# Performance work log

Hardware: AMD Instinct MI355X
Metric: run time of the kernel (lower is better)

Reference implementation:

```python
import jax, jax.numpy as jnp
import numpy as np

DIM = 1024
FF = 4096
BATCH = 4
SEQ = 2048
EPS = 1e-5


def setup_inputs() -> dict:
    key = jax.random.key(0)
    ks = jax.random.split(key, 8)
    x = jax.random.normal(ks[0], (BATCH, SEQ, DIM), dtype=jnp.float32)
    # phazor init: exp(2j*pi*arange(dim)/dim) * |randn(dim)|
    ang = 2.0 * np.pi * jnp.arange(DIM, dtype=jnp.float32) / DIM
    mag = jnp.abs(jax.random.normal(ks[1], (DIM,), dtype=jnp.float32))
    phazor_re = mag * jnp.cos(ang)
    phazor_im = mag * jnp.sin(ang)
    last_re = jax.random.normal(ks[2], (DIM,), dtype=jnp.float32)
    last_im = jax.random.normal(ks[3], (DIM,), dtype=jnp.float32)
    w1 = jax.random.normal(ks[4], (FF, DIM), dtype=jnp.float32) * DIM ** -0.5
    b1 = jnp.zeros((FF,), dtype=jnp.float32)
    w2 = jax.random.normal(ks[5], (DIM, FF), dtype=jnp.float32) * FF ** -0.5
    b2 = jnp.zeros((DIM,), dtype=jnp.float32)
    return {
        'x': x,
        'ln1_w': jnp.ones((DIM,), jnp.float32), 'ln1_b': jnp.zeros((DIM,), jnp.float32),
        'ln2_w': jnp.ones((DIM,), jnp.float32), 'ln2_b': jnp.zeros((DIM,), jnp.float32),
        'sc_lin': jnp.ones((DIM,), jnp.float32),
        'phazor_re': phazor_re, 'phazor_im': phazor_im,
        'last_re': last_re, 'last_im': last_im,
        'w1': w1, 'b1': b1, 'w2': w2, 'b2': b2,
    }


def _layer_norm(x, w, b):
    mu = jnp.mean(x, axis=-1, keepdims=True)
    var = jnp.mean(jnp.square(x - mu), axis=-1, keepdims=True)
    return (x - mu) * jax.lax.rsqrt(var + EPS) * w + b


def _sconv(x, phazor_re, phazor_im, last_re, last_im):
    B, L, D = x.shape
    dtype = x.dtype
    xc = x.astype(jnp.complex64)
    p_raw = phazor_re + 1j * phazor_im
    # tanh(|p|) * exp(i*angle(p))
    p = (jnp.tanh(jnp.abs(p_raw)) * jnp.exp(1j * jnp.angle(p_raw))).astype(jnp.complex64)
    t = jnp.arange(L)[:, None]
    prog = jnp.power(p[None, :], t)            # [L, D] complex
    filt_fft = jnp.fft.fft(prog, n=2 * L, axis=0)   # [2L, D]
    x_fft = jnp.fft.fft(xc, n=2 * L, axis=1)        # [B, 2L, D]
    conv = jnp.fft.ifft(filt_fft[None] * x_fft, axis=1)[:, :L]  # [B, L, D]
    last = (last_re + 1j * last_im)[None, None, :]  # [1,1,D] broadcast over batch
    conv_with_past = conv + last * prog[None] * p[None, None]
    return conv_with_past.real.astype(dtype)


def reference(x, ln1_w, ln1_b, ln2_w, ln2_b, sc_lin,
              phazor_re, phazor_im, last_re, last_im,
              w1, b1, w2, b2):
    # SConv branch
    x_res = x
    h = _layer_norm(x, ln1_w, ln1_b)
    h = jax.nn.silu(h)
    h = _sconv(h, phazor_re, phazor_im, last_re, last_im)
    h = h * sc_lin
    x = h + x_res
    # FFN branch
    x_res = x
    h = _layer_norm(x, ln2_w, ln2_b)
    h = jax.nn.silu(jnp.einsum('bld,fd->blf', h, w1) + b1)
    h = jnp.einsum('blf,df->bld', h, w2) + b2
    return h + x_res
```

## Files before the change

kernel.cpp:

```cpp
#include <hip/hip_runtime.h>
#include <cmath>


#define DIMD 1024
#define FFD  4096
#define BATCH 4
#define SEQL 2048
#define MROWS (BATCH*SEQL)
#define EPSF 1e-5f
#define CHUNKS 32
#define CLEN (SEQL/CHUNKS)

typedef __attribute__((ext_vector_type(8)))  _Float16 half8;
typedef __attribute__((ext_vector_type(4)))  _Float16 half4;
typedef __attribute__((ext_vector_type(4)))  float    floatx4;
typedef __attribute__((ext_vector_type(16))) float    floatx16;

#define ST_OFF   0u
#define E_OFF    33554432u
#define SIN_OFF  34603008u
#define H2_OFF   35651584u
#define W1H_OFF  52428800u
#define W2H_OFF  60817408u
#define Y1_OFF   69206016u

__device__ __forceinline__ void load_lds16(const _Float16* g, _Float16* l) {
    __builtin_amdgcn_global_load_lds(
        (const __attribute__((address_space(1))) unsigned int*)g,
        (__attribute__((address_space(3))) unsigned int*)l,
        16, 0, 0);
}

__global__ __launch_bounds__(256)
void cast_f32_f16(const float* __restrict__ src, _Float16* __restrict__ dst) {
    int i = (blockIdx.x * 256 + threadIdx.x) * 4;
    float4 v = *(const float4*)(src + i);
    half4 o;
    o.x = (_Float16)v.x; o.y = (_Float16)v.y; o.z = (_Float16)v.z; o.w = (_Float16)v.w;
    *(half4*)(dst + i) = o;
}

__global__ __launch_bounds__(256)
void ln_stats(const float* __restrict__ x, float2* __restrict__ st) {
    const size_t row = blockIdx.x;
    const int tid = threadIdx.x;
    float4 v = *(const float4*)(x + row * DIMD + tid * 4);
    float s = (v.x + v.y) + (v.z + v.w);
    float q = (v.x * v.x + v.y * v.y) + (v.z * v.z + v.w * v.w);
    #pragma unroll
    for (int off = 32; off; off >>= 1) {
        s += __shfl_down(s, off, 64);
        q += __shfl_down(q, off, 64);
    }
    __shared__ float red[8];
    if (!(tid & 63)) { red[tid >> 6] = s; red[4 + (tid >> 6)] = q; }
    __syncthreads();
    if (tid == 0) {
        s = (red[0] + red[1]) + (red[2] + red[3]);
        q = (red[4] + red[5]) + (red[6] + red[7]);
        const float mu = s * (1.f / DIMD);
        const float rs = rsqrtf(q * (1.f / DIMD) - mu * mu + EPSF);
        st[row] = make_float2(mu, rs);
    }
}

__global__ __launch_bounds__(256)
void ln_kernel(const float* __restrict__ x, const float* __restrict__ w,
               const float* __restrict__ b, _Float16* __restrict__ oh) {
    const size_t row = blockIdx.x;
    const int tid = threadIdx.x;
    float4 v = *(const float4*)(x + row * DIMD + tid * 4);
    float s = (v.x + v.y) + (v.z + v.w);
    float q = (v.x * v.x + v.y * v.y) + (v.z * v.z + v.w * v.w);
    #pragma unroll
    for (int off = 32; off; off >>= 1) {
        s += __shfl_down(s, off, 64);
        q += __shfl_down(q, off, 64);
    }
    __shared__ float red[8];
    if (!(tid & 63)) { red[tid >> 6] = s; red[4 + (tid >> 6)] = q; }
    __syncthreads();
    s = (red[0] + red[1]) + (red[2] + red[3]);
    q = (red[4] + red[5]) + (red[6] + red[7]);
    const float mu = s * (1.f / DIMD);
    const float rs = rsqrtf(q * (1.f / DIMD) - mu * mu + EPSF);
    float4 wv = *(const float4*)(w + tid * 4);
    float4 bv = *(const float4*)(b + tid * 4);
    half4 hv;
    hv.x = (_Float16)((v.x - mu) * rs * wv.x + bv.x);
    hv.y = (_Float16)((v.y - mu) * rs * wv.y + bv.y);
    hv.z = (_Float16)((v.z - mu) * rs * wv.z + bv.z);
    hv.w = (_Float16)((v.w - mu) * rs * wv.w + bv.w);
    *(half4*)(oh + row * DIMD + tid * 4) = hv;
}

__device__ __forceinline__ void get_p(const float* pre, const float* pim, int d,
                                      float& pr, float& pi) {
    float re = pre[d], im = pim[d];
    float r = sqrtf(re * re + im * im);
    float t = tanhf(r) / fmaxf(r, 1e-30f);
    pr = re * t; pi = im * t;
}

__device__ __forceinline__ float ln_silu(float xv, float2 st, float wd, float bd) {
    float o = (xv - st.x) * st.y * wd + bd;
    return o / (1.f + __expf(-o));
}

__global__ __launch_bounds__(256)
void scan_partial(const float* __restrict__ x, const float2* __restrict__ st,
                  const float* __restrict__ lw, const float* __restrict__ lb,
                  const float* __restrict__ pre, const float* __restrict__ pim,
                  float2* __restrict__ e) {
    const int d = blockIdx.x * 256 + threadIdx.x;
    const int c = blockIdx.y;
    const int bb = blockIdx.z;
    float pr, pi; get_p(pre, pim, d, pr, pi);
    const float wd = lw[d], bd = lb[d];
    float sr = 0.f, si = 0.f;
    const size_t row0 = (size_t)bb * SEQL + (size_t)c * CLEN;
    #pragma unroll 4
    for (int j = 0; j < CLEN; ++j) {
        float xv = x[(row0 + j) * DIMD + d];
        float2 sj = st[row0 + j];
        float hv = ln_silu(xv, sj, wd, bd);
        float nr = pr * sr - pi * si + hv;
        float ni = pr * si + pi * sr;
        sr = nr; si = ni;
    }
    e[((size_t)bb * CHUNKS + c) * DIMD + d] = make_float2(sr, si);
}

__global__ __launch_bounds__(256)
void scan_combine(const float2* __restrict__ e, const float* __restrict__ pre,
                  const float* __restrict__ pim, const float* __restrict__ lre,
                  const float* __restrict__ lim, float2* __restrict__ sv) {
    const int d = blockIdx.x * 256 + threadIdx.x;
    const int bb = blockIdx.y;
    float pr, pi; get_p(pre, pim, d, pr, pi);
    float qr = pr, qi = pi;
    #pragma unroll
    for (int s = 0; s < 6; ++s) {
        float nr = qr * qr - qi * qi;
        float ni = 2.f * qr * qi;
        qr = nr; qi = ni;
    }
    float sr = lre[d], si = lim[d];
    for (int c = 0; c < CHUNKS; ++c) {
        sv[((size_t)bb * CHUNKS + c) * DIMD + d] = make_float2(sr, si);
        float2 ec = e[((size_t)bb * CHUNKS + c) * DIMD + d];
        float nr = qr * sr - qi * si + ec.x;
        float ni = qr * si + qi * sr + ec.y;
        sr = nr; si = ni;
    }
}

__global__ __launch_bounds__(256)
void scan_final(const float* __restrict__ x, const float2* __restrict__ st,
                const float* __restrict__ lw, const float* __restrict__ lb,
                const float* __restrict__ pre, const float* __restrict__ pim,
                const float* __restrict__ sc, const float2* __restrict__ sv,
                float* __restrict__ x2) {
    const int d = blockIdx.x * 256 + threadIdx.x;
    const int c = blockIdx.y;
    const int bb = blockIdx.z;
    float pr, pi; get_p(pre, pim, d, pr, pi);
    const float wd = lw[d], bd = lb[d];
    float2 s0 = sv[((size_t)bb * CHUNKS + c) * DIMD + d];
    float sr = s0.x, si = s0.y;
    const float scd = sc[d];
    const size_t row0 = (size_t)bb * SEQL + (size_t)c * CLEN;
    #pragma unroll 4
    for (int j = 0; j < CLEN; ++j) {
        float xv = x[(row0 + j) * DIMD + d];
        float2 sj = st[row0 + j];
        float hv = ln_silu(xv, sj, wd, bd);
        float nr = pr * sr - pi * si + hv;
        float ni = pr * si + pi * sr;
        sr = nr; si = ni;
        x2[(row0 + j) * DIMD + d] = xv + scd * sr;
    }
}

#define GBM 128
#define GBN 128
#define GBK 64

template<int NCOLS>
__global__ __launch_bounds__(256)
void gemm1_32(const _Float16* __restrict__ A, const _Float16* __restrict__ W,
              const float* __restrict__ bias, _Float16* __restrict__ out_h,
              int N, int K) {
    __shared__ _Float16 As[GBM * GBK];
    __shared__ _Float16 Bs[GBN * GBK];
    const int tid  = threadIdx.x;
    const int lane = tid & 63;
    const int wave = tid >> 6;
    const int wm = (wave >> 1) * 64;
    const int wn = (wave & 1) * 64;
    const int n  = blockIdx.y * gridDim.x + blockIdx.x;
    const int xc = n & 7, ii = n >> 3;
    const size_t m0 = (size_t)(xc + ((ii / NCOLS) << 3)) * GBM;
    const size_t n0 = (size_t)(ii % NCOLS) * GBN;
    const int r32 = lane & 31;
    const int kg  = lane >> 5;

    const int srow = wave * 32 + (lane >> 3);
    const int ccp  = ((lane & 7) ^ (lane >> 3)) * 8;
    const _Float16* ag = A + (m0 + srow) * (size_t)K + ccp;
    const _Float16* wg = W + (n0 + srow) * (size_t)K + ccp;
    _Float16* asl = &As[(wave * 32) * GBK];
    _Float16* bsl = &Bs[(wave * 32) * GBK];

    floatx16 acc[2][2] = {};

    for (int k0 = 0; k0 < K; k0 += GBK) {
        #pragma unroll
        for (int t = 0; t < 4; ++t) {
            load_lds16(ag + k0 + (size_t)(t * 8) * K, asl + t * 8 * GBK);
            load_lds16(wg + k0 + (size_t)(t * 8) * K, bsl + t * 8 * GBK);
        }
        __syncthreads();
        #pragma unroll
        for (int ks = 0; ks < 4; ++ks) {
            const int slot = (((ks << 1) | kg) ^ (r32 & 7)) * 8;
            half8 af0 = *(const half8*)(&As[(wm +      r32) * GBK + slot]);
            half8 af1 = *(const half8*)(&As[(wm + 32 + r32) * GBK + slot]);
            half8 bf0 = *(const half8*)(&Bs[(wn +      r32) * GBK + slot]);
            half8 bf1 = *(const half8*)(&Bs[(wn + 32 + r32) * GBK + slot]);
            acc[0][0] = __builtin_amdgcn_mfma_f32_32x32x16_f16(af0, bf0, acc[0][0], 0, 0, 0);
            acc[0][1] = __builtin_amdgcn_mfma_f32_32x32x16_f16(af0, bf1, acc[0][1], 0, 0, 0);
            acc[1][0] = __builtin_amdgcn_mfma_f32_32x32x16_f16(af1, bf0, acc[1][0], 0, 0, 0);
            acc[1][1] = __builtin_amdgcn_mfma_f32_32x32x16_f16(af1, bf1, acc[1][1], 0, 0, 0);
        }
        __syncthreads();
    }

    #pragma unroll
    for (int ib = 0; ib < 2; ++ib) {
        #pragma unroll
        for (int jb = 0; jb < 2; ++jb) {
            const size_t gn = n0 + wn + jb * 32 + r32;
            const float bb = bias[gn];
            #pragma unroll
            for (int r = 0; r < 16; ++r) {
                const size_t gm = m0 + wm + ib * 32 + (r & 3) + 8 * (r >> 2) + 4 * kg;
                float v = acc[ib][jb][r] + bb;
                float sl = v / (1.f + __expf(-v));
                out_h[gm * (size_t)N + gn] = (_Float16)sl;
            }
        }
    }
}

template<int NCOLS>
__global__ __launch_bounds__(256)
void gemm2_16(const _Float16* __restrict__ A, const _Float16* __restrict__ W,
              const float* __restrict__ bias, const float* __restrict__ resid,
              float* __restrict__ out_f, int N, int K) {
    __shared__ _Float16 As[GBM * GBK];
    __shared__ _Float16 Bs[GBN * GBK];
    const int tid  = threadIdx.x;
    const int lane = tid & 63;
    const int wave = tid >> 6;
    const int wm = (wave >> 1) * 64;
    const int wn = (wave & 1) * 64;
    const int n  = blockIdx.y * gridDim.x + blockIdx.x;
    const int xc = n & 7, ii = n >> 3;
    const size_t m0 = (size_t)(xc + ((ii / NCOLS) << 3)) * GBM;
    const size_t n0 = (size_t)(ii % NCOLS) * GBN;
    const int fr = lane & 15;
    const int quad = lane >> 4;

    const int srow = wave * 32 + (lane >> 3);
    const int ccp  = ((lane & 7) ^ (lane >> 3)) * 8;
    const _Float16* ag = A + (m0 + srow) * (size_t)K + ccp;
    const _Float16* wg = W + (n0 + srow) * (size_t)K + ccp;
    _Float16* asl = &As[(wave * 32) * GBK];
    _Float16* bsl = &Bs[(wave * 32) * GBK];

    floatx4 acc[4][4] = {};

    for (int k0 = 0; k0 < K; k0 += GBK) {
        #pragma unroll
        for (int t = 0; t < 4; ++t) {
            load_lds16(ag + k0 + (size_t)(t * 8) * K, asl + t * 8 * GBK);
            load_lds16(wg + k0 + (size_t)(t * 8) * K, bsl + t * 8 * GBK);
        }
        __syncthreads();
        #pragma unroll
        for (int kk = 0; kk < GBK; kk += 32) {
            half8 af[4], bf[4];
            #pragma unroll
            for (int i = 0; i < 4; ++i) {
                const int slot = (((kk >> 3) + quad) ^ (fr & 7)) * 8;
                af[i] = *(const half8*)(&As[(wm + i * 16 + fr) * GBK + slot]);
                bf[i] = *(const half8*)(&Bs[(wn + i * 16 + fr) * GBK + slot]);
            }
            #pragma unroll
            for (int i = 0; i < 4; ++i)
                #pragma unroll
                for (int j = 0; j < 4; ++j)
                    acc[i][j] = __builtin_amdgcn_mfma_f32_16x16x32_f16(
                        af[i], bf[j], acc[i][j], 0, 0, 0);
        }
        __syncthreads();
    }

    #pragma unroll
    for (int i = 0; i < 4; ++i) {
        #pragma unroll
        for (int j = 0; j < 4; ++j) {
            #pragma unroll
            for (int r = 0; r < 4; ++r) {
                const size_t gm = m0 + wm + i * 16 + quad * 4 + r;
                const size_t gn = n0 + wn + j * 16 + fr;
                float v = acc[i][j][r] + bias[gn];
                out_f[gm * (size_t)N + gn] = v + resid[gm * (size_t)N + gn];
            }
        }
    }
}

extern "C" void kernel_launch(void* const* d_in, const int* in_sizes, int n_in,
                              void* d_out, int out_size, void* d_ws, size_t ws_size,
                              hipStream_t stream) {
    const float* x    = (const float*)d_in[0];
    const float* ln1w = (const float*)d_in[1];
    const float* ln1b = (const float*)d_in[2];
    const float* ln2w = (const float*)d_in[3];
    const float* ln2b = (const float*)d_in[4];
    const float* sc   = (const float*)d_in[5];
    const float* pre  = (const float*)d_in[6];
    const float* pim  = (const float*)d_in[7];
    const float* lre  = (const float*)d_in[8];
    const float* lim  = (const float*)d_in[9];
    const float* w1   = (const float*)d_in[10];
    const float* b1   = (const float*)d_in[11];
    const float* w2   = (const float*)d_in[12];
    const float* b2   = (const float*)d_in[13];

    char* ws = (char*)d_ws;
    float2*     st  = (float2*)(ws + ST_OFF);
    float2*     e   = (float2*)(ws + E_OFF);
    float2*     sv  = (float2*)(ws + SIN_OFF);
    _Float16*   h2  = (_Float16*)(ws + H2_OFF);
    _Float16*   w1h = (_Float16*)(ws + W1H_OFF);
    _Float16*   w2h = (_Float16*)(ws + W2H_OFF);
    _Float16*   y1  = (_Float16*)(ws + Y1_OFF);
    float*      x2  = (float*)d_out;
    float*      outp = (float*)d_out;

    cast_f32_f16<<<dim3(FFD * DIMD / 1024), 256, 0, stream>>>(w1, w1h);
    cast_f32_f16<<<dim3(FFD * DIMD / 1024), 256, 0, stream>>>(w2, w2h);
    ln_stats<<<dim3(MROWS), 256, 0, stream>>>(x, st);
    scan_partial<<<dim3(DIMD / 256, CHUNKS, BATCH), 256, 0, stream>>>(
        x, st, ln1w, ln1b, pre, pim, e);
    scan_combine<<<dim3(DIMD / 256, BATCH), 256, 0, stream>>>(
        e, pre, pim, lre, lim, sv);
    scan_final<<<dim3(DIMD / 256, CHUNKS, BATCH), 256, 0, stream>>>(
        x, st, ln1w, ln1b, pre, pim, sc, sv, x2);
    ln_kernel<<<dim3(MROWS), 256, 0, stream>>>(x2, ln2w, ln2b, h2);
    gemm1_32<32><<<dim3(FFD / GBN, MROWS / GBM), 256, 0, stream>>>(
        h2, w1h, b1, y1, FFD, DIMD);
    gemm2_16<8><<<dim3(DIMD / GBN, MROWS / GBM), 256, 0, stream>>>(
        y1, w2h, b2, x2, outp, DIMD, FFD);
}
```

Baseline: 353.7 us.

## Merge prep kernels and fold scan combine into final scan pass

The two weight-cast kernels and the LN-stats kernel become one launch, with each block picking its job from its index. The separate scan_combine kernel is removed. Each scan_final block now recomputes its chunk's starting state by walking the earlier chunk carries itself. This removes two kernel launches and the write/read round-trip of the intermediate state buffer, in exchange for redundant carry computation (up to 31 steps per block).

```diff
diff --git a/kernel.cpp b/kernel.cpp
--- a/kernel.cpp
+++ b/kernel.cpp
@@ -10,6 +10,7 @@
 #define EPSF 1e-5f
 #define CHUNKS 32
 #define CLEN (SEQL/CHUNKS)
+#define CAST_BLKS (FFD*DIMD/1024)
 
 typedef __attribute__((ext_vector_type(8)))  _Float16 half8;
 typedef __attribute__((ext_vector_type(4)))  _Float16 half4;
@@ -18,7 +19,6 @@
 
 #define ST_OFF   0u
 #define E_OFF    33554432u
-#define SIN_OFF  34603008u
 #define H2_OFF   35651584u
 #define W1H_OFF  52428800u
 #define W2H_OFF  60817408u
@@ -32,35 +32,43 @@
 }
 
 __global__ __launch_bounds__(256)
-void cast_f32_f16(const float* __restrict__ src, _Float16* __restrict__ dst) {
-    int i = (blockIdx.x * 256 + threadIdx.x) * 4;
-    float4 v = *(const float4*)(src + i);
-    half4 o;
-    o.x = (_Float16)v.x; o.y = (_Float16)v.y; o.z = (_Float16)v.z; o.w = (_Float16)v.w;
-    *(half4*)(dst + i) = o;
-}
-
-__global__ __launch_bounds__(256)
-void ln_stats(const float* __restrict__ x, float2* __restrict__ st) {
-    const size_t row = blockIdx.x;
+void prep(const float* __restrict__ x, float2* __restrict__ st,
+          const float* __restrict__ w1, _Float16* __restrict__ w1h,
+          const float* __restrict__ w2, _Float16* __restrict__ w2h) {
+    const int bid = blockIdx.x;
     const int tid = threadIdx.x;
-    float4 v = *(const float4*)(x + row * DIMD + tid * 4);
-    float s = (v.x + v.y) + (v.z + v.w);
-    float q = (v.x * v.x + v.y * v.y) + (v.z * v.z + v.w * v.w);
-    #pragma unroll
-    for (int off = 32; off; off >>= 1) {
-        s += __shfl_down(s, off, 64);
-        q += __shfl_down(q, off, 64);
-    }
-    __shared__ float red[8];
-    if (!(tid & 63)) { red[tid >> 6] = s; red[4 + (tid >> 6)] = q; }
-    __syncthreads();
-    if (tid == 0) {
-        s = (red[0] + red[1]) + (red[2] + red[3]);
-        q = (red[4] + red[5]) + (red[6] + red[7]);
-        const float mu = s * (1.f / DIMD);
-        const float rs = rsqrtf(q * (1.f / DIMD) - mu * mu + EPSF);
-        st[row] = make_float2(mu, rs);
+    if (bid < MROWS) {
+        const size_t row = bid;
+        float4 v = *(const float4*)(x + row * DIMD + tid * 4);
+        float s = (v.x + v.y) + (v.z + v.w);
+        float q = (v.x * v.x + v.y * v.y) + (v.z * v.z + v.w * v.w);
+        #pragma unroll
+        for (int off = 32; off; off >>= 1) {
+            s += __shfl_down(s, off, 64);
+            q += __shfl_down(q, off, 64);
+        }
+        __shared__ float red[8];
+        if (!(tid & 63)) { red[tid >> 6] = s; red[4 + (tid >> 6)] = q; }
+        __syncthreads();
+        if (tid == 0) {
+            s = (red[0] + red[1]) + (red[2] + red[3]);
+            q = (red[4] + red[5]) + (red[6] + red[7]);
+            const float mu = s * (1.f / DIMD);
+            const float rs = rsqrtf(q * (1.f / DIMD) - mu * mu + EPSF);
+            st[row] = make_float2(mu, rs);
+        }
+    } else {
+        int b = bid - MROWS;
+        const float* src;
+        _Float16* dst;
+        if (b < CAST_BLKS) { src = w1; dst = w1h; }
+        else { b -= CAST_BLKS; src = w2; dst = w2h; }
+        int i = (b * 256 + tid) * 4;
+        float4 v = *(const float4*)(src + i);
+        half4 o;
+        o.x = (_Float16)v.x; o.y = (_Float16)v.y;
+        o.z = (_Float16)v.z; o.w = (_Float16)v.w;
+        *(half4*)(dst + i) = o;
     }
 }
 
@@ -132,12 +140,17 @@
 }
 
 __global__ __launch_bounds__(256)
-void scan_combine(const float2* __restrict__ e, const float* __restrict__ pre,
-                  const float* __restrict__ pim, const float* __restrict__ lre,
-                  const float* __restrict__ lim, float2* __restrict__ sv) {
+void scan_final(const float* __restrict__ x, const float2* __restrict__ st,
+                const float* __restrict__ lw, const float* __restrict__ lb,
+                const float* __restrict__ pre, const float* __restrict__ pim,
+                const float* __restrict__ sc, const float* __restrict__ lre,
+                const float* __restrict__ lim, const float2* __restrict__ e,
+                float* __restrict__ x2) {
     const int d = blockIdx.x * 256 + threadIdx.x;
-    const int bb = blockIdx.y;
+    const int c = blockIdx.y;
+    const int bb = blockIdx.z;
     float pr, pi; get_p(pre, pim, d, pr, pi);
+    const float wd = lw[d], bd = lb[d];
     float qr = pr, qi = pi;
     #pragma unroll
     for (int s = 0; s < 6; ++s) {
@@ -146,28 +159,13 @@
         qr = nr; qi = ni;
     }
     float sr = lre[d], si = lim[d];
-    for (int c = 0; c < CHUNKS; ++c) {
-        sv[((size_t)bb * CHUNKS + c) * DIMD + d] = make_float2(sr, si);
-        float2 ec = e[((size_t)bb * CHUNKS + c) * DIMD + d];
+    const float2* ep = e + (size_t)bb * CHUNKS * DIMD + d;
+    for (int cc = 0; cc < c; ++cc) {
+        float2 ec = ep[(size_t)cc * DIMD];
         float nr = qr * sr - qi * si + ec.x;
         float ni = qr * si + qi * sr + ec.y;
         sr = nr; si = ni;
     }
-}
-
-__global__ __launch_bounds__(256)
-void scan_final(const float* __restrict__ x, const float2* __restrict__ st,
-                const float* __restrict__ lw, const float* __restrict__ lb,
-                const float* __restrict__ pre, const float* __restrict__ pim,
-                const float* __restrict__ sc, const float2* __restrict__ sv,
-                float* __restrict__ x2) {
-    const int d = blockIdx.x * 256 + threadIdx.x;
-    const int c = blockIdx.y;
-    const int bb = blockIdx.z;
-    float pr, pi; get_p(pre, pim, d, pr, pi);
-    const float wd = lw[d], bd = lb[d];
-    float2 s0 = sv[((size_t)bb * CHUNKS + c) * DIMD + d];
-    float sr = s0.x, si = s0.y;
     const float scd = sc[d];
     const size_t row0 = (size_t)bb * SEQL + (size_t)c * CLEN;
     #pragma unroll 4
@@ -343,7 +341,6 @@
     char* ws = (char*)d_ws;
     float2*     st  = (float2*)(ws + ST_OFF);
     float2*     e   = (float2*)(ws + E_OFF);
-    float2*     sv  = (float2*)(ws + SIN_OFF);
     _Float16*   h2  = (_Float16*)(ws + H2_OFF);
     _Float16*   w1h = (_Float16*)(ws + W1H_OFF);
     _Float16*   w2h = (_Float16*)(ws + W2H_OFF);
@@ -351,15 +348,12 @@
     float*      x2  = (float*)d_out;
     float*      outp = (float*)d_out;
 
-    cast_f32_f16<<<dim3(FFD * DIMD / 1024), 256, 0, stream>>>(w1, w1h);
-    cast_f32_f16<<<dim3(FFD * DIMD / 1024), 256, 0, stream>>>(w2, w2h);
-    ln_stats<<<dim3(MROWS), 256, 0, stream>>>(x, st);
+    prep<<<dim3(MROWS + 2 * CAST_BLKS), 256, 0, stream>>>(
+        x, st, w1, w1h, w2, w2h);
     scan_partial<<<dim3(DIMD / 256, CHUNKS, BATCH), 256, 0, stream>>>(
         x, st, ln1w, ln1b, pre, pim, e);
-    scan_combine<<<dim3(DIMD / 256, BATCH), 256, 0, stream>>>(
-        e, pre, pim, lre, lim, sv);
     scan_final<<<dim3(DIMD / 256, CHUNKS, BATCH), 256, 0, stream>>>(
-        x, st, ln1w, ln1b, pre, pim, sc, sv, x2);
+        x, st, ln1w, ln1b, pre, pim, sc, lre, lim, e, x2);
     ln_kernel<<<dim3(MROWS), 256, 0, stream>>>(x2, ln2w, ln2b, h2);
     gemm1_32<32><<<dim3(FFD / GBN, MROWS / GBM), 256, 0, stream>>>(
         h2, w1h, b1, y1, FFD, DIMD);
```

New measurement: 345.1 us. -2.4%, faster.
